# Kernel tuning notes

Hardware: AMD Instinct MI355X
Metric: run time of the kernel (lower is better)

Reference implementation:

```python
import jax, jax.numpy as jnp
import numpy as np

B, K, D, H, L = 128, 128, 768, 8, 4
HD = D // H
FF = 4 * D
SIM = D // 4
BOOST = 0.3
SCALE = HD ** -0.5
EPS = 1e-5


def _ln(x, g, b):
    m = x.mean(-1, keepdims=True)
    v = ((x - m) ** 2).mean(-1, keepdims=True)
    return (x - m) * jax.lax.rsqrt(v + EPS) * g + b


def setup_inputs() -> dict:
    key = jax.random.key(0)
    ks = jax.random.split(key, 10)
    def n(k, shape, s=0.02):
        return jax.random.normal(k, shape, dtype=jnp.float32) * s
    return {
        'slots': jax.random.normal(ks[0], (B, K, D), dtype=jnp.float32),
        'pos_emb': n(ks[1], (1, K, D)),
        'Wq': n(ks[2], (L, D, D)),
        'Wk': n(ks[3], (L, D, D)),
        'Wv': n(ks[4], (L, D, D)),
        'Wo': n(ks[5], (L, D, D)),
        'bo': jnp.zeros((L, D), jnp.float32),
        'Wsim': n(ks[6], (L, D, SIM)),
        'g1': jnp.ones((L, D), jnp.float32),
        'b1': jnp.zeros((L, D), jnp.float32),
        'g2': jnp.ones((L, D), jnp.float32),
        'b2': jnp.zeros((L, D), jnp.float32),
        'Wff1': n(ks[7], (L, D, FF)),
        'bff1': jnp.zeros((L, FF), jnp.float32),
        'Wff2': n(ks[8], (L, FF, D)),
        'bff2': jnp.zeros((L, D), jnp.float32),
        'gf': jnp.ones((D,), jnp.float32),
        'bf': jnp.zeros((D,), jnp.float32),
    }


def reference(slots, pos_emb, Wq, Wk, Wv, Wo, bo, Wsim, g1, b1, g2, b2,
              Wff1, bff1, Wff2, bff2, gf, bf):
    x = slots + pos_emb  # K == max_slots -> full pos table
    for l in range(L):
        # --- similarity-biased multi-head self-attention (pre-norm) ---
        nx = _ln(x, g1[l], b1[l])
        q = (nx @ Wq[l]).reshape(B, K, H, HD)
        k = (nx @ Wk[l]).reshape(B, K, H, HD)
        v = (nx @ Wv[l]).reshape(B, K, H, HD)
        scores = jnp.einsum('bqhd,bkhd->bhqk', q, k) * SCALE  # [B,H,K,K]
        s = nx @ Wsim[l]  # [B,K,D/4]
        s = s / jnp.maximum(jnp.linalg.norm(s, axis=-1, keepdims=True), 1e-12)
        sim = jnp.einsum('bqc,bkc->bqk', s, s)  # cosine similarity matrix
        scores = scores + BOOST * sim[:, None, :, :]
        a = jax.nn.softmax(scores, axis=-1)
        o = jnp.einsum('bhqk,bkhd->bqhd', a, v).reshape(B, K, D)
        x = x + (o @ Wo[l] + bo[l])
        # --- feed-forward (pre-norm) ---
        nx = _ln(x, g2[l], b2[l])
        h = jax.nn.gelu(nx @ Wff1[l] + bff1[l], approximate=False)
        x = x + (h @ Wff2[l] + bff2[l])
    return _ln(x, gf, bf)
```

## Files before the change

### kernel.cpp

```cpp
#include <hip/hip_runtime.h>

typedef unsigned short u16;
typedef unsigned int u32;
typedef float f32x4 __attribute__((ext_vector_type(4)));
typedef __bf16 bf16x8 __attribute__((ext_vector_type(8)));

static constexpr int D = 768, FFD = 3072, SIMC = 192, NH = 8, HD = 96;
static constexpr int B = 128, K = 128, M = B * K, NL = 4;
static constexpr int QKVW = 2560;
static constexpr int SIMOFF = 2304;
static constexpr float QSCALE = 0.14724502f;
static constexpr float SBOOST2 = 0.6578821f;
static constexpr float EPS_F = 1e-5f;

__device__ __forceinline__ float bf2f(u16 u) {
  union { u32 i; float f; } v; v.i = ((u32)u) << 16; return v.f;
}
__device__ __forceinline__ u16 f2bf(float f) {
  union { float f; u32 i; } v; v.f = f;
  u32 u = v.i;
  u32 r = (u + 0x7FFFu + ((u >> 16) & 1u)) >> 16;
  return (u16)r;
}
__device__ __forceinline__ u32 pack2(float a, float b) {
  return (u32)f2bf(a) | ((u32)f2bf(b) << 16);
}

__device__ __forceinline__ float fast_gelu(float x) {
  float u2 = x * (2.3020585f + 0.102944f * x * x);
  float e = __builtin_amdgcn_exp2f(u2);
  float r = __builtin_amdgcn_rcpf(1.0f + e);
  return x - x * r;
}

__device__ __forceinline__ void gload16(const void* g, void* l) {
  __builtin_amdgcn_global_load_lds(
      (const __attribute__((address_space(1))) void*)g,
      (__attribute__((address_space(3))) void*)l, 16, 0, 0);
}

template <bool OUT_BF16>
__global__ __launch_bounds__(256) void ln_kernel(
    const u16* __restrict__ x, const float* __restrict__ g,
    const float* __restrict__ b, void* __restrict__ out) {
  int row = blockIdx.x * 4 + (threadIdx.x >> 6);
  int lane = threadIdx.x & 63;
  const u16* xr = x + (size_t)row * D;
  uint4 a = *(const uint4*)(xr + lane * 8);
  uint2 c = *(const uint2*)(xr + 512 + lane * 4);
  float v[12];
  u32 aa[4] = {a.x, a.y, a.z, a.w};
#pragma unroll
  for (int j = 0; j < 4; ++j) {
    v[2 * j] = bf2f((u16)(aa[j] & 0xffffu));
    v[2 * j + 1] = bf2f((u16)(aa[j] >> 16));
  }
  u32 cc[2] = {c.x, c.y};
#pragma unroll
  for (int j = 0; j < 2; ++j) {
    v[8 + 2 * j] = bf2f((u16)(cc[j] & 0xffffu));
    v[9 + 2 * j] = bf2f((u16)(cc[j] >> 16));
  }
  float s = 0.f;
#pragma unroll
  for (int j = 0; j < 12; ++j) s += v[j];
#pragma unroll
  for (int off = 32; off > 0; off >>= 1) s += __shfl_xor(s, off, 64);
  float mean = s * (1.0f / D);
  float sq = 0.f;
#pragma unroll
  for (int j = 0; j < 12; ++j) { float d0 = v[j] - mean; sq += d0 * d0; }
#pragma unroll
  for (int off = 32; off > 0; off >>= 1) sq += __shfl_xor(sq, off, 64);
  float rs = rsqrtf(sq * (1.0f / D) + EPS_F);
  float4 g0 = *(const float4*)(g + lane * 8);
  float4 g1 = *(const float4*)(g + lane * 8 + 4);
  float4 g2 = *(const float4*)(g + 512 + lane * 4);
  float4 b0 = *(const float4*)(b + lane * 8);
  float4 b1 = *(const float4*)(b + lane * 8 + 4);
  float4 b2 = *(const float4*)(b + 512 + lane * 4);
  float gv[12] = {g0.x, g0.y, g0.z, g0.w, g1.x, g1.y, g1.z, g1.w,
                  g2.x, g2.y, g2.z, g2.w};
  float bv[12] = {b0.x, b0.y, b0.z, b0.w, b1.x, b1.y, b1.z, b1.w,
                  b2.x, b2.y, b2.z, b2.w};
  float y[12];
#pragma unroll
  for (int j = 0; j < 12; ++j) y[j] = (v[j] - mean) * rs * gv[j] + bv[j];
  if (OUT_BF16) {
    u16* o = (u16*)out + (size_t)row * D;
    uint4 oa = {pack2(y[0], y[1]), pack2(y[2], y[3]),
                pack2(y[4], y[5]), pack2(y[6], y[7])};
    uint2 oc = {pack2(y[8], y[9]), pack2(y[10], y[11])};
    *(uint4*)(o + lane * 8) = oa;
    *(uint2*)(o + 512 + lane * 4) = oc;
  } else {
    float* o = (float*)out + (size_t)row * D;
    *(float4*)(o + lane * 8) = {y[0], y[1], y[2], y[3]};
    *(float4*)(o + lane * 8 + 4) = {y[4], y[5], y[6], y[7]};
    *(float4*)(o + 512 + lane * 4) = {y[8], y[9], y[10], y[11]};
  }
}

struct WAll {
  const float *wq, *wk, *wv, *wo, *wsim, *wff1, *wff2;
  u16 *tA, *tB, *tC, *tD;
  const float *slots, *pos;
  u16* x;
};
__global__ __launch_bounds__(256) void wconv_all_kernel(WAll p, float qscale) {
  __shared__ u16 t[32][33];
  int bid = blockIdx.x;
  int tid = threadIdx.x;
  if (bid >= 28224) {
    int i8 = ((bid - 28224) * 256 + tid) * 8;
    int m = i8 / D;
    int d = i8 - m * D;
    int pd = (m & (K - 1)) * D + d;
    float4 s0 = *(const float4*)(p.slots + i8);
    float4 s1 = *(const float4*)(p.slots + i8 + 4);
    float4 p0 = *(const float4*)(p.pos + pd);
    float4 p1 = *(const float4*)(p.pos + pd + 4);
    uint4 o = {pack2(s0.x + p0.x, s0.y + p0.y), pack2(s0.z + p0.z, s0.w + p0.w),
               pack2(s1.x + p1.x, s1.y + p1.y), pack2(s1.z + p1.z, s1.w + p1.w)};
    *(uint4*)(p.x + i8) = o;
    return;
  }
  int l = bid / 7056, b = bid - l * 7056;
  const float* W; u16* Wt; int N, Kd, n0, k0;
  float sc = 1.0f;
  if (b < 2304) {
    int z = b / 576, rem = b - z * 576;
    N = 768; Kd = 768;
    n0 = (rem % 24) * 32; k0 = (rem / 24) * 32;
    if (z == 0) { W = p.wq + (size_t)l * 589824; Wt = p.tA + (size_t)l * 1966080; sc = qscale; }
    else if (z == 1) { W = p.wk + (size_t)l * 589824; Wt = p.tA + (size_t)l * 1966080 + 589824; }
    else if (z == 2) { W = p.wv + (size_t)l * 589824; Wt = p.tA + (size_t)l * 1966080 + 1179648; }
    else { W = p.wo + (size_t)l * 589824; Wt = p.tB + (size_t)l * 589824; }
  } else if (b < 2448) {
    int rem = b - 2304;
    W = p.wsim + (size_t)l * 147456;
    Wt = p.tA + (size_t)l * 1966080 + (size_t)SIMOFF * 768;
    N = SIMC; Kd = 768;
    n0 = (rem % 6) * 32; k0 = (rem / 6) * 32;
  } else if (b < 4752) {
    int rem = b - 2448;
    W = p.wff1 + (size_t)l * 2359296; Wt = p.tC + (size_t)l * 2359296;
    N = FFD; Kd = 768;
    n0 = (rem % 96) * 32; k0 = (rem / 96) * 32;
  } else {
    int rem = b - 4752;
    W = p.wff2 + (size_t)l * 2359296; Wt = p.tD + (size_t)l * 2359296;
    N = 768; Kd = FFD;
    n0 = (rem % 24) * 32; k0 = (rem / 24) * 32;
  }
  int c = tid & 31, r4 = tid >> 5;
#pragma unroll
  for (int i = 0; i < 4; ++i) {
    int r = r4 + i * 8;
    t[r][c] = f2bf(W[(size_t)(k0 + r) * N + n0 + c] * sc);
  }
  __syncthreads();
#pragma unroll
  for (int i = 0; i < 4; ++i) {
    int r = r4 + i * 8;
    Wt[(size_t)(n0 + r) * Kd + k0 + c] = t[c][r];
  }
}

template <bool BIAS, bool GELU_, bool RESID>
__global__ __launch_bounds__(512, 2) void gemm256_kernel(
    const u16* __restrict__ A, const u16* __restrict__ Bt,
    const float* __restrict__ bias, const u16* __restrict__ resid,
    u16* __restrict__ Cout, int N, int Kdim, int NBX) {
  __shared__ u16 lds[65536];
  int tid = threadIdx.x;
  int w = tid >> 6, lane = tid & 63;
  int wm = w >> 2, wn = w & 3;
  int lr = lane & 15, lg = lane >> 4;

  int nwg = gridDim.x;
  int cpx = nwg >> 3;
  int swz = (blockIdx.x & 7) * cpx + (blockIdx.x >> 3);
  int bx = swz % NBX, by = swz / NBX;
  int n0 = bx << 8, m0 = by << 8;

  int scol = ((lane & 7) ^ (lane >> 3)) << 3;
  size_t aOff = (size_t)((w << 4) + (lane >> 3)) * Kdim + scol;
  u16* ldsU = lds;

  auto stageA = [&](int buf, int h, int t) {
    const u16* g = A + (size_t)(m0 + (h << 7)) * Kdim + ((size_t)t << 6) + aOff;
    u16* l = ldsU + buf * 32768 + h * 8192 + (w << 10);
    gload16(g, l);
    gload16(g + ((size_t)Kdim << 3), l + 512);
  };
  auto stageB = [&](int buf, int h, int t) {
    const u16* g = Bt + (size_t)(n0 + (h << 7)) * Kdim + ((size_t)t << 6) + aOff;
    u16* l = ldsU + buf * 32768 + 16384 + h * 8192 + (w << 10);
    gload16(g, l);
    gload16(g + ((size_t)Kdim << 3), l + 512);
  };

  const u16* lA0p = ldsU;
  const u16* lB0p = ldsU + 16384;
  const u16* lA1p = ldsU + 32768;
  const u16* lB1p = ldsU + 49152;
  int arow = (wm * 128 + lr) * 64;
  int brow = (wn * 64 + lr) * 64;
  int swz0 = (((lg * 16)) ^ ((lr & 7) << 4)) >> 1;
  int swz1 = ((64 + lg * 16) ^ ((lr & 7) << 4)) >> 1;

  f32x4 acc[8][4] = {};
  bf16x8 ar[2][4], br[2][4];

#define READ_A_KS(BASE, MSEG, KS)                                            \
  do {                                                                       \
    _Pragma("unroll") for (int mm = 0; mm < 4; ++mm) {                       \
      const u16* p_ = (BASE) + arow + ((MSEG) * 64 + mm * 16) * 64;          \
      ar[KS][mm] = *(const bf16x8*)(p_ + ((KS) ? swz1 : swz0));              \
    }                                                                        \
  } while (0)
#define READ_B_KS(BASE, NSEG, KS)                                            \
  do {                                                                       \
    _Pragma("unroll") for (int nn = 0; nn < 2; ++nn) {                       \
      const u16* p_ = (BASE) + brow + ((NSEG) * 32 + nn * 16) * 64;          \
      br[KS][(NSEG) * 2 + nn] = *(const bf16x8*)(p_ + ((KS) ? swz1 : swz0)); \
    }                                                                        \
  } while (0)
#define MFMA_Q(MSEG, NSEG)                                                   \
  do {                                                                       \
    __builtin_amdgcn_s_setprio(1);                                           \
    _Pragma("unroll") for (int ks = 0; ks < 2; ++ks)                         \
      _Pragma("unroll") for (int mm = 0; mm < 4; ++mm)                       \
        _Pragma("unroll") for (int nn = 0; nn < 2; ++nn)                     \
          acc[(MSEG) * 4 + mm][(NSEG) * 2 + nn] =                            \
              __builtin_amdgcn_mfma_f32_16x16x32_bf16(                       \
                  ar[ks][mm], br[ks][(NSEG) * 2 + nn],                       \
                  acc[(MSEG) * 4 + mm][(NSEG) * 2 + nn], 0, 0, 0);           \
    __builtin_amdgcn_s_setprio(0);                                           \
  } while (0)
#define PSYNC()                                                              \
  do {                                                                       \
    __builtin_amdgcn_sched_barrier(0);                                       \
    asm volatile("s_waitcnt lgkmcnt(0)" ::: "memory");                       \
    __builtin_amdgcn_s_barrier();                                            \
    __builtin_amdgcn_sched_barrier(0);                                       \
  } while (0)
#define PSYNC_V(N)                                                           \
  do {                                                                       \
    __builtin_amdgcn_sched_barrier(0);                                       \
    asm volatile("s_waitcnt vmcnt(" #N ") lgkmcnt(0)" ::: "memory");         \
    __builtin_amdgcn_s_barrier();                                            \
    __builtin_amdgcn_sched_barrier(0);                                       \
  } while (0)

  int NK = Kdim >> 6, NI = NK >> 1;
  stageA(0, 0, 0); stageA(0, 1, 0); stageB(0, 0, 0); stageB(0, 1, 0);
  stageB(1, 0, 1); stageB(1, 1, 1);
  asm volatile("s_waitcnt vmcnt(4)" ::: "memory");
  __builtin_amdgcn_s_barrier();
  __builtin_amdgcn_sched_barrier(0);

  for (int i = 0; i < NI; ++i) {
    int t1 = 2 * i + 1, t2 = 2 * i + 2, t3 = 2 * i + 3;
    bool last = (i == NI - 1);
    stageA(1, 0, t1); stageA(1, 1, t1);
    READ_A_KS(lA0p, 0, 0); READ_B_KS(lB0p, 0, 0); READ_B_KS(lB0p, 1, 0);
    READ_A_KS(lA0p, 0, 1); READ_B_KS(lB0p, 0, 1); READ_B_KS(lB0p, 1, 1);
    MFMA_Q(0, 0); MFMA_Q(0, 1);
    PSYNC();
    if (!last) { stageB(0, 0, t2); stageB(0, 1, t2); }
    READ_A_KS(lA0p, 1, 0); READ_A_KS(lA0p, 1, 1);
    MFMA_Q(1, 0); MFMA_Q(1, 1);
    if (last) PSYNC_V(0);
    else      PSYNC_V(4);
    if (!last) { stageA(0, 0, t2); stageA(0, 1, t2); }
    READ_A_KS(lA1p, 0, 0); READ_B_KS(lB1p, 0, 0); READ_B_KS(lB1p, 1, 0);
    READ_A_KS(lA1p, 0, 1); READ_B_KS(lB1p, 0, 1); READ_B_KS(lB1p, 1, 1);
    MFMA_Q(0, 0); MFMA_Q(0, 1);
    PSYNC();
    if (!last) { stageB(1, 0, t3); stageB(1, 1, t3); }
    READ_A_KS(lA1p, 1, 0); READ_A_KS(lA1p, 1, 1);
    MFMA_Q(1, 0); MFMA_Q(1, 1);
    if (last) PSYNC();
    else      PSYNC_V(4);
  }

#pragma unroll
  for (int m = 0; m < 8; ++m) {
#pragma unroll
    for (int n = 0; n < 4; ++n) {
      int col = n0 + wn * 64 + n * 16 + lr;
      float bv = BIAS ? bias[col] : 0.0f;
#pragma unroll
      for (int r = 0; r < 4; ++r) {
        int row = m0 + wm * 128 + m * 16 + lg * 4 + r;
        float v = acc[m][n][r];
        if (BIAS) v += bv;
        if (GELU_) v = fast_gelu(v);
        if (RESID) v += bf2f(resid[(size_t)row * N + col]);
        Cout[(size_t)row * N + col] = f2bf(v);
      }
    }
  }
#undef READ_A_KS
#undef READ_B_KS
#undef MFMA_Q
#undef PSYNC
#undef PSYNC_V
}

__global__ __launch_bounds__(256) void simpre_kernel(
    const u16* __restrict__ qkvb, u16* __restrict__ psim) {
  __shared__ u16 sln[128][200];
  int b = blockIdx.x, tid = threadIdx.x;
  {
    int row = tid >> 1, half = tid & 1;
    const u16* sr = qkvb + ((size_t)(b * K + row)) * QKVW + SIMOFF + half * 96;
    u16 v[96];
    float sq = 0.f;
#pragma unroll
    for (int j = 0; j < 12; ++j) {
      uint4 u4 = *(const uint4*)(sr + j * 8);
      u32 uu[4] = {u4.x, u4.y, u4.z, u4.w};
#pragma unroll
      for (int t = 0; t < 4; ++t) {
        v[j * 8 + 2 * t] = (u16)(uu[t] & 0xffffu);
        v[j * 8 + 2 * t + 1] = (u16)(uu[t] >> 16);
      }
    }
#pragma unroll
    for (int j = 0; j < 96; ++j) { float f = bf2f(v[j]); sq += f * f; }
    sq += __shfl_xor(sq, 1, 64);
    float inv = SBOOST2 / fmaxf(sqrtf(sq), 1e-12f);
#pragma unroll
    for (int j = 0; j < 96; ++j) sln[row][half * 96 + j] = f2bf(bf2f(v[j]) * inv);
  }
  __syncthreads();
  int w = tid >> 6, lane = tid & 63;
  int lr = lane & 15, lg = lane >> 4;
  int q0 = 32 * w;
  f32x4 accs[2][8] = {};
#pragma unroll
  for (int ks = 0; ks < 6; ++ks) {
    bf16x8 af[2];
#pragma unroll
    for (int m = 0; m < 2; ++m)
      af[m] = *(const bf16x8*)(&sln[q0 + 16 * m + lr][ks * 32 + lg * 8]);
#pragma unroll
    for (int n = 0; n < 8; ++n) {
      bf16x8 bf = *(const bf16x8*)(&sln[16 * n + lr][ks * 32 + lg * 8]);
#pragma unroll
      for (int m = 0; m < 2; ++m)
        accs[m][n] = __builtin_amdgcn_mfma_f32_16x16x32_bf16(af[m], bf, accs[m][n], 0, 0, 0);
    }
  }
  u16* pb = psim + (size_t)b * K * K;
#pragma unroll
  for (int m = 0; m < 2; ++m)
#pragma unroll
    for (int n = 0; n < 8; ++n)
#pragma unroll
      for (int r = 0; r < 4; ++r)
        pb[(size_t)(q0 + 16 * m + 4 * lg + r) * K + 16 * n + lr] = f2bf(accs[m][n][r]);
}

__global__ __launch_bounds__(256) void attn_kernel(
    const u16* __restrict__ qkv, const u16* __restrict__ psim,
    u16* __restrict__ ob) {
  __shared__ u16 Vt[96][136];
  __shared__ u16 Pl[4][32][136];
  int bh = blockIdx.x, b = bh >> 3, h = bh & 7;
  int tid = threadIdx.x, w = tid >> 6, lane = tid & 63;
  int lr = lane & 15, lg = lane >> 4;
  const u16* qb = qkv + (size_t)b * K * QKVW + h * HD;
  const u16* kb = qb + D;
  const u16* vb = qb + 2 * D;
  for (int idx = tid; idx < 128 * 12; idx += 256) {
    int r = idx / 12, db = idx - r * 12;
    uint4 v4 = *(const uint4*)(vb + (size_t)r * QKVW + db * 8);
    u32 vv[4] = {v4.x, v4.y, v4.z, v4.w};
#pragma unroll
    for (int j = 0; j < 4; ++j) {
      Vt[db * 8 + 2 * j][r] = (u16)(vv[j] & 0xffffu);
      Vt[db * 8 + 2 * j + 1][r] = (u16)(vv[j] >> 16);
    }
  }
  u16* Kl = &Pl[0][0][0];
  for (int idx = tid; idx < 128 * 12; idx += 256) {
    int r = idx / 12, db = idx - r * 12;
    *(uint4*)(Kl + r * 104 + db * 8) = *(const uint4*)(kb + (size_t)r * QKVW + db * 8);
  }
  __syncthreads();
  int q0 = 32 * w;
  f32x4 accs[2][8] = {};
#pragma unroll
  for (int ks = 0; ks < 3; ++ks) {
    bf16x8 af[2];
#pragma unroll
    for (int m = 0; m < 2; ++m)
      af[m] = *(const bf16x8*)(qb + (size_t)(q0 + 16 * m + lr) * QKVW + ks * 32 + lg * 8);
#pragma unroll
    for (int n = 0; n < 8; ++n) {
      bf16x8 bf = *(const bf16x8*)(Kl + (16 * n + lr) * 104 + ks * 32 + lg * 8);
#pragma unroll
      for (int m = 0; m < 2; ++m)
        accs[m][n] = __builtin_amdgcn_mfma_f32_16x16x32_bf16(af[m], bf, accs[m][n], 0, 0, 0);
    }
  }
  __syncthreads();
  const u16* pb = psim + (size_t)b * K * K;
#pragma unroll
  for (int m = 0; m < 2; ++m)
#pragma unroll
    for (int n = 0; n < 8; ++n)
#pragma unroll
      for (int r = 0; r < 4; ++r)
        accs[m][n][r] += bf2f(pb[(size_t)(q0 + 16 * m + 4 * lg + r) * 128 + 16 * n + lr]);
#pragma unroll
  for (int m = 0; m < 2; ++m) {
    float mx[4] = {-3e38f, -3e38f, -3e38f, -3e38f};
#pragma unroll
    for (int n = 0; n < 8; ++n)
#pragma unroll
      for (int r = 0; r < 4; ++r) mx[r] = fmaxf(mx[r], accs[m][n][r]);
#pragma unroll
    for (int r = 0; r < 4; ++r) {
      mx[r] = fmaxf(mx[r], __shfl_xor(mx[r], 1, 64));
      mx[r] = fmaxf(mx[r], __shfl_xor(mx[r], 2, 64));
      mx[r] = fmaxf(mx[r], __shfl_xor(mx[r], 4, 64));
      mx[r] = fmaxf(mx[r], __shfl_xor(mx[r], 8, 64));
    }
    float sm[4] = {0.f, 0.f, 0.f, 0.f};
#pragma unroll
    for (int n = 0; n < 8; ++n)
#pragma unroll
      for (int r = 0; r < 4; ++r) {
        float e = __builtin_amdgcn_exp2f(accs[m][n][r] - mx[r]);
        accs[m][n][r] = e;
        sm[r] += e;
      }
#pragma unroll
    for (int r = 0; r < 4; ++r) {
      sm[r] += __shfl_xor(sm[r], 1, 64);
      sm[r] += __shfl_xor(sm[r], 2, 64);
      sm[r] += __shfl_xor(sm[r], 4, 64);
      sm[r] += __shfl_xor(sm[r], 8, 64);
    }
    float inv[4];
#pragma unroll
    for (int r = 0; r < 4; ++r) inv[r] = 1.0f / sm[r];
#pragma unroll
    for (int n = 0; n < 8; ++n)
#pragma unroll
      for (int r = 0; r < 4; ++r)
        Pl[w][16 * m + 4 * lg + r][16 * n + lr] = f2bf(accs[m][n][r] * inv[r]);
  }
  __syncthreads();
  f32x4 acco[2][6] = {};
#pragma unroll
  for (int ks = 0; ks < 4; ++ks) {
    bf16x8 pa[2];
#pragma unroll
    for (int m = 0; m < 2; ++m)
      pa[m] = *(const bf16x8*)(&Pl[w][16 * m + lr][ks * 32 + lg * 8]);
#pragma unroll
    for (int n = 0; n < 6; ++n) {
      bf16x8 bv = *(const bf16x8*)(&Vt[16 * n + lr][ks * 32 + lg * 8]);
#pragma unroll
      for (int m = 0; m < 2; ++m)
        acco[m][n] = __builtin_amdgcn_mfma_f32_16x16x32_bf16(pa[m], bv, acco[m][n], 0, 0, 0);
    }
  }
  u16* obb = ob + (size_t)b * K * D + h * HD;
#pragma unroll
  for (int m = 0; m < 2; ++m)
#pragma unroll
    for (int n = 0; n < 6; ++n)
#pragma unroll
      for (int r = 0; r < 4; ++r)
        obb[(size_t)(q0 + 16 * m + 4 * lg + r) * D + 16 * n + lr] = f2bf(acco[m][n][r]);
}

extern "C" void kernel_launch(void* const* d_in, const int* in_sizes, int n_in,
                              void* d_out, int out_size, void* d_ws, size_t ws_size,
                              hipStream_t stream) {
  (void)in_sizes; (void)n_in; (void)out_size;
  const float* slots = (const float*)d_in[0];
  const float* pos   = (const float*)d_in[1];
  const float* Wq    = (const float*)d_in[2];
  const float* Wk    = (const float*)d_in[3];
  const float* Wv    = (const float*)d_in[4];
  const float* Wo    = (const float*)d_in[5];
  const float* bo    = (const float*)d_in[6];
  const float* Wsim  = (const float*)d_in[7];
  const float* g1    = (const float*)d_in[8];
  const float* b1    = (const float*)d_in[9];
  const float* g2    = (const float*)d_in[10];
  const float* b2    = (const float*)d_in[11];
  const float* Wff1  = (const float*)d_in[12];
  const float* bff1  = (const float*)d_in[13];
  const float* Wff2  = (const float*)d_in[14];
  const float* bff2  = (const float*)d_in[15];
  const float* gf    = (const float*)d_in[16];
  const float* bfin  = (const float*)d_in[17];

  char* p = (char*)d_ws;
  u16*   x    = (u16*)p;   p += (size_t)M * D * 2;
  u16*   nx   = (u16*)p;   p += (size_t)M * D * 2;
  u16*   qkvb = (u16*)p;   p += (size_t)M * QKVW * 2;
  u16*   ob   = (u16*)p;   p += (size_t)M * D * 2;
  u16*   psim = (u16*)p;   p += (size_t)B * K * K * 2;
  u16*   wtA4 = (u16*)p;   p += (size_t)4 * QKVW * D * 2;
  u16*   wtB4 = (u16*)p;   p += (size_t)4 * D * D * 2;
  u16*   wtC4 = (u16*)p;   p += (size_t)4 * FFD * D * 2;
  u16*   wtD4 = (u16*)p;   p += (size_t)4 * D * FFD * 2;
  if ((size_t)(p - (char*)d_ws) > ws_size) return;
  u16* hb = qkvb;

  WAll wp = {Wq, Wk, Wv, Wo, Wsim, Wff1, Wff2, wtA4, wtB4, wtC4, wtD4,
             slots, pos, x};
  wconv_all_kernel<<<28224 + 6144, 256, 0, stream>>>(wp, QSCALE);

  int nbx_qkv = QKVW / 256, nwg_qkv = nbx_qkv * (M / 256);
  int nbx_o   = D / 256,    nwg_o   = nbx_o * (M / 256);
  int nbx_f1  = FFD / 256,  nwg_f1  = nbx_f1 * (M / 256);

  for (int l = 0; l < NL; ++l) {
    ln_kernel<true><<<M / 4, 256, 0, stream>>>(x, g1 + l * D, b1 + l * D, nx);
    gemm256_kernel<false, false, false><<<nwg_qkv, 512, 0, stream>>>(
        nx, wtA4 + (size_t)l * QKVW * D, nullptr, nullptr, qkvb, QKVW, D, nbx_qkv);
    simpre_kernel<<<B, 256, 0, stream>>>(qkvb, psim);
    attn_kernel<<<B * NH, 256, 0, stream>>>(qkvb, psim, ob);
    gemm256_kernel<true, false, true><<<nwg_o, 512, 0, stream>>>(
        ob, wtB4 + (size_t)l * D * D, bo + l * D, x, x, D, D, nbx_o);
    ln_kernel<true><<<M / 4, 256, 0, stream>>>(x, g2 + l * D, b2 + l * D, nx);
    gemm256_kernel<true, true, false><<<nwg_f1, 512, 0, stream>>>(
        nx, wtC4 + (size_t)l * FFD * D, bff1 + l * FFD, nullptr, hb, FFD, D, nbx_f1);
    gemm256_kernel<true, false, true><<<nwg_o, 512, 0, stream>>>(
        hb, wtD4 + (size_t)l * D * FFD, bff2 + l * D, x, x, D, FFD, nbx_o);
  }
  ln_kernel<false><<<M / 4, 256, 0, stream>>>(x, gf, bfin, d_out);
}
```

Measured before the change: 1.325 ms.

## Replace 256x256 GEMM tile with simpler 128x256 double-buffered tile

Rewrites the GEMM kernel to use a 128x256 output tile with a K-step of 32 and a simple two-buffer LDS pipeline, replacing the hand-scheduled 256x256 ping-pong schedule. LDS use drops from 128KB to 48KB and the launch bound asks for 4 workgroups per CU, so more blocks can be resident and the grid has twice as many workgroups. In exchange, each tile reuses its loaded data less, takes a full barrier and vmcnt(0) wait every 32-wide K step, and loses the interleaved load/MFMA scheduling.

```diff
diff --git a/kernel.cpp b/kernel.cpp
--- a/kernel.cpp
+++ b/kernel.cpp
@@ -168,11 +168,11 @@
 }
 
 template <bool BIAS, bool GELU_, bool RESID>
-__global__ __launch_bounds__(512, 2) void gemm256_kernel(
+__global__ __launch_bounds__(512, 4) void gemm_kernel(
     const u16* __restrict__ A, const u16* __restrict__ Bt,
     const float* __restrict__ bias, const u16* __restrict__ resid,
     u16* __restrict__ Cout, int N, int Kdim, int NBX) {
-  __shared__ u16 lds[65536];
+  __shared__ u16 lds[24576];
   int tid = threadIdx.x;
   int w = tid >> 6, lane = tid & 63;
   int wm = w >> 2, wn = w & 3;
@@ -182,119 +182,74 @@
   int cpx = nwg >> 3;
   int swz = (blockIdx.x & 7) * cpx + (blockIdx.x >> 3);
   int bx = swz % NBX, by = swz / NBX;
-  int n0 = bx << 8, m0 = by << 8;
-
-  int scol = ((lane & 7) ^ (lane >> 3)) << 3;
-  size_t aOff = (size_t)((w << 4) + (lane >> 3)) * Kdim + scol;
-  u16* ldsU = lds;
-
-  auto stageA = [&](int buf, int h, int t) {
-    const u16* g = A + (size_t)(m0 + (h << 7)) * Kdim + ((size_t)t << 6) + aOff;
-    u16* l = ldsU + buf * 32768 + h * 8192 + (w << 10);
-    gload16(g, l);
-    gload16(g + ((size_t)Kdim << 3), l + 512);
+  int n0 = bx << 8, m0 = by << 7;
+
+  int unitA = (w << 6) + lane;
+  int rowA = unitA >> 2;
+  int colA = ((unitA & 3) ^ (rowA & 3)) << 3;
+  const u16* gA = A + (size_t)(m0 + rowA) * Kdim + colA;
+  int unitB0 = (w << 6) + lane;
+  int rowB0 = unitB0 >> 2;
+  int colB0 = ((unitB0 & 3) ^ (rowB0 & 3)) << 3;
+  const u16* gB0 = Bt + (size_t)(n0 + rowB0) * Kdim + colB0;
+  int unitB1 = 512 + (w << 6) + lane;
+  int rowB1 = unitB1 >> 2;
+  int colB1 = ((unitB1 & 3) ^ (rowB1 & 3)) << 3;
+  const u16* gB1 = Bt + (size_t)(n0 + rowB1) * Kdim + colB1;
+  int wbase = w << 9;
+
+  auto stage = [&](int buf, int t) {
+    gload16(gA + t * 32, lds + buf * 4096 + wbase);
+    gload16(gB0 + t * 32, lds + 8192 + buf * 8192 + wbase);
+    gload16(gB1 + t * 32, lds + 8192 + buf * 8192 + 4096 + wbase);
   };
-  auto stageB = [&](int buf, int h, int t) {
-    const u16* g = Bt + (size_t)(n0 + (h << 7)) * Kdim + ((size_t)t << 6) + aOff;
-    u16* l = ldsU + buf * 32768 + 16384 + h * 8192 + (w << 10);
-    gload16(g, l);
-    gload16(g + ((size_t)Kdim << 3), l + 512);
-  };
-
-  const u16* lA0p = ldsU;
-  const u16* lB0p = ldsU + 16384;
-  const u16* lA1p = ldsU + 32768;
-  const u16* lB1p = ldsU + 49152;
-  int arow = (wm * 128 + lr) * 64;
-  int brow = (wn * 64 + lr) * 64;
-  int swz0 = (((lg * 16)) ^ ((lr & 7) << 4)) >> 1;
-  int swz1 = ((64 + lg * 16) ^ ((lr & 7) << 4)) >> 1;
-
-  f32x4 acc[8][4] = {};
-  bf16x8 ar[2][4], br[2][4];
-
-#define READ_A_KS(BASE, MSEG, KS)                                            \
-  do {                                                                       \
-    _Pragma("unroll") for (int mm = 0; mm < 4; ++mm) {                       \
-      const u16* p_ = (BASE) + arow + ((MSEG) * 64 + mm * 16) * 64;          \
-      ar[KS][mm] = *(const bf16x8*)(p_ + ((KS) ? swz1 : swz0));              \
-    }                                                                        \
-  } while (0)
-#define READ_B_KS(BASE, NSEG, KS)                                            \
-  do {                                                                       \
-    _Pragma("unroll") for (int nn = 0; nn < 2; ++nn) {                       \
-      const u16* p_ = (BASE) + brow + ((NSEG) * 32 + nn * 16) * 64;          \
-      br[KS][(NSEG) * 2 + nn] = *(const bf16x8*)(p_ + ((KS) ? swz1 : swz0)); \
-    }                                                                        \
-  } while (0)
-#define MFMA_Q(MSEG, NSEG)                                                   \
-  do {                                                                       \
-    __builtin_amdgcn_s_setprio(1);                                           \
-    _Pragma("unroll") for (int ks = 0; ks < 2; ++ks)                         \
-      _Pragma("unroll") for (int mm = 0; mm < 4; ++mm)                       \
-        _Pragma("unroll") for (int nn = 0; nn < 2; ++nn)                     \
-          acc[(MSEG) * 4 + mm][(NSEG) * 2 + nn] =                            \
-              __builtin_amdgcn_mfma_f32_16x16x32_bf16(                       \
-                  ar[ks][mm], br[ks][(NSEG) * 2 + nn],                       \
-                  acc[(MSEG) * 4 + mm][(NSEG) * 2 + nn], 0, 0, 0);           \
-    __builtin_amdgcn_s_setprio(0);                                           \
-  } while (0)
-#define PSYNC()                                                              \
-  do {                                                                       \
-    __builtin_amdgcn_sched_barrier(0);                                       \
-    asm volatile("s_waitcnt lgkmcnt(0)" ::: "memory");                       \
-    __builtin_amdgcn_s_barrier();                                            \
-    __builtin_amdgcn_sched_barrier(0);                                       \
-  } while (0)
-#define PSYNC_V(N)                                                           \
-  do {                                                                       \
-    __builtin_amdgcn_sched_barrier(0);                                       \
-    asm volatile("s_waitcnt vmcnt(" #N ") lgkmcnt(0)" ::: "memory");         \
-    __builtin_amdgcn_s_barrier();                                            \
-    __builtin_amdgcn_sched_barrier(0);                                       \
-  } while (0)
-
-  int NK = Kdim >> 6, NI = NK >> 1;
-  stageA(0, 0, 0); stageA(0, 1, 0); stageB(0, 0, 0); stageB(0, 1, 0);
-  stageB(1, 0, 1); stageB(1, 1, 1);
-  asm volatile("s_waitcnt vmcnt(4)" ::: "memory");
+
+  int swzu = (lg ^ (lr & 3)) << 3;
+  int arow = (wm * 64 + lr) * 32 + swzu;
+  int brow = (wn * 64 + lr) * 32 + swzu;
+
+  f32x4 acc[4][4] = {};
+  bf16x8 ar[4], br[4];
+
+  int NK = Kdim >> 5;
+  stage(0, 0);
+  asm volatile("s_waitcnt vmcnt(0)" ::: "memory");
   __builtin_amdgcn_s_barrier();
   __builtin_amdgcn_sched_barrier(0);
 
-  for (int i = 0; i < NI; ++i) {
-    int t1 = 2 * i + 1, t2 = 2 * i + 2, t3 = 2 * i + 3;
-    bool last = (i == NI - 1);
-    stageA(1, 0, t1); stageA(1, 1, t1);
-    READ_A_KS(lA0p, 0, 0); READ_B_KS(lB0p, 0, 0); READ_B_KS(lB0p, 1, 0);
-    READ_A_KS(lA0p, 0, 1); READ_B_KS(lB0p, 0, 1); READ_B_KS(lB0p, 1, 1);
-    MFMA_Q(0, 0); MFMA_Q(0, 1);
-    PSYNC();
-    if (!last) { stageB(0, 0, t2); stageB(0, 1, t2); }
-    READ_A_KS(lA0p, 1, 0); READ_A_KS(lA0p, 1, 1);
-    MFMA_Q(1, 0); MFMA_Q(1, 1);
-    if (last) PSYNC_V(0);
-    else      PSYNC_V(4);
-    if (!last) { stageA(0, 0, t2); stageA(0, 1, t2); }
-    READ_A_KS(lA1p, 0, 0); READ_B_KS(lB1p, 0, 0); READ_B_KS(lB1p, 1, 0);
-    READ_A_KS(lA1p, 0, 1); READ_B_KS(lB1p, 0, 1); READ_B_KS(lB1p, 1, 1);
-    MFMA_Q(0, 0); MFMA_Q(0, 1);
-    PSYNC();
-    if (!last) { stageB(1, 0, t3); stageB(1, 1, t3); }
-    READ_A_KS(lA1p, 1, 0); READ_A_KS(lA1p, 1, 1);
-    MFMA_Q(1, 0); MFMA_Q(1, 1);
-    if (last) PSYNC();
-    else      PSYNC_V(4);
-  }
-
-#pragma unroll
-  for (int m = 0; m < 8; ++m) {
+  for (int t = 0; t < NK; ++t) {
+    int cur = t & 1;
+    if (t + 1 < NK) stage(cur ^ 1, t + 1);
+    const u16* lA = lds + cur * 4096;
+    const u16* lB = lds + 8192 + cur * 8192;
+#pragma unroll
+    for (int m = 0; m < 4; ++m)
+      ar[m] = *(const bf16x8*)(lA + arow + m * 512);
+#pragma unroll
+    for (int n = 0; n < 4; ++n)
+      br[n] = *(const bf16x8*)(lB + brow + n * 512);
+    __builtin_amdgcn_s_setprio(1);
+#pragma unroll
+    for (int m = 0; m < 4; ++m)
+#pragma unroll
+      for (int n = 0; n < 4; ++n)
+        acc[m][n] = __builtin_amdgcn_mfma_f32_16x16x32_bf16(ar[m], br[n], acc[m][n], 0, 0, 0);
+    __builtin_amdgcn_s_setprio(0);
+    __builtin_amdgcn_sched_barrier(0);
+    asm volatile("s_waitcnt vmcnt(0) lgkmcnt(0)" ::: "memory");
+    __builtin_amdgcn_s_barrier();
+    __builtin_amdgcn_sched_barrier(0);
+  }
+
+#pragma unroll
+  for (int m = 0; m < 4; ++m) {
 #pragma unroll
     for (int n = 0; n < 4; ++n) {
       int col = n0 + wn * 64 + n * 16 + lr;
       float bv = BIAS ? bias[col] : 0.0f;
 #pragma unroll
       for (int r = 0; r < 4; ++r) {
-        int row = m0 + wm * 128 + m * 16 + lg * 4 + r;
+        int row = m0 + wm * 64 + m * 16 + lg * 4 + r;
         float v = acc[m][n][r];
         if (BIAS) v += bv;
         if (GELU_) v = fast_gelu(v);
@@ -303,11 +258,6 @@
       }
     }
   }
-#undef READ_A_KS
-#undef READ_B_KS
-#undef MFMA_Q
-#undef PSYNC
-#undef PSYNC_V
 }
 
 __global__ __launch_bounds__(256) void simpre_kernel(
@@ -522,22 +472,22 @@
              slots, pos, x};
   wconv_all_kernel<<<28224 + 6144, 256, 0, stream>>>(wp, QSCALE);
 
-  int nbx_qkv = QKVW / 256, nwg_qkv = nbx_qkv * (M / 256);
-  int nbx_o   = D / 256,    nwg_o   = nbx_o * (M / 256);
-  int nbx_f1  = FFD / 256,  nwg_f1  = nbx_f1 * (M / 256);
+  int nbx_qkv = QKVW / 256, nwg_qkv = nbx_qkv * (M / 128);
+  int nbx_o   = D / 256,    nwg_o   = nbx_o * (M / 128);
+  int nbx_f1  = FFD / 256,  nwg_f1  = nbx_f1 * (M / 128);
 
   for (int l = 0; l < NL; ++l) {
     ln_kernel<true><<<M / 4, 256, 0, stream>>>(x, g1 + l * D, b1 + l * D, nx);
-    gemm256_kernel<false, false, false><<<nwg_qkv, 512, 0, stream>>>(
+    gemm_kernel<false, false, false><<<nwg_qkv, 512, 0, stream>>>(
         nx, wtA4 + (size_t)l * QKVW * D, nullptr, nullptr, qkvb, QKVW, D, nbx_qkv);
     simpre_kernel<<<B, 256, 0, stream>>>(qkvb, psim);
     attn_kernel<<<B * NH, 256, 0, stream>>>(qkvb, psim, ob);
-    gemm256_kernel<true, false, true><<<nwg_o, 512, 0, stream>>>(
+    gemm_kernel<true, false, true><<<nwg_o, 512, 0, stream>>>(
         ob, wtB4 + (size_t)l * D * D, bo + l * D, x, x, D, D, nbx_o);
     ln_kernel<true><<<M / 4, 256, 0, stream>>>(x, g2 + l * D, b2 + l * D, nx);
-    gemm256_kernel<true, true, false><<<nwg_f1, 512, 0, stream>>>(
+    gemm_kernel<true, true, false><<<nwg_f1, 512, 0, stream>>>(
         nx, wtC4 + (size_t)l * FFD * D, bff1 + l * FFD, nullptr, hb, FFD, D, nbx_f1);
-    gemm256_kernel<true, false, true><<<nwg_o, 512, 0, stream>>>(
+    gemm_kernel<true, false, true><<<nwg_o, 512, 0, stream>>>(
         hb, wtD4 + (size_t)l * D * FFD, bff2 + l * D, x, x, D, FFD, nbx_o);
   }
   ln_kernel<false><<<M / 4, 256, 0, stream>>>(x, gf, bfin, d_out);
```

Result: slower. 1.413 ms (+6.7%).
